# Performance work log

Hardware: AMD Instinct MI355X
Metric: run time of the kernel (lower is better)

Reference implementation:

```python
import jax, jax.numpy as jnp
import numpy as np

N = 200000   # nodes
E = 6400000  # edges (avg degree 32)
D = 128      # input feature dim
H = 10       # hidden dim (hardcoded in module)


def setup_inputs() -> dict:
    key = jax.random.key(0)
    ks = jax.random.split(key, 16)
    x = jax.random.normal(ks[0], (N, D), dtype=jnp.float32)
    edge_index = jax.random.randint(ks[1], (2, E), 0, N, dtype=jnp.int32)

    def lin(k, fan_in, fan_out):
        s = 1.0 / np.sqrt(fan_in)
        k1, k2 = jax.random.split(k)
        W = jax.random.uniform(k1, (fan_in, fan_out), jnp.float32, -s, s)
        b = jax.random.uniform(k2, (fan_out,), jnp.float32, -s, s)
        return W, b

    W1, b1 = lin(ks[2], D, H)    # conv_succ1
    W2, b2 = lin(ks[3], H, H)    # conv_succ2
    Wp, bp = lin(ks[4], H, H)    # conv_pred1
    W3, b3 = lin(ks[5], H, H)    # conv_succ3
    Wo, bo = lin(ks[6], H, 1)    # conv_probs (conv_output)
    Wdn, bdn = lin(ks[7], H, 1)  # do_nothing
    Wv, bv = lin(ks[8], H, 1)    # value
    return {"x": x, "edge_index": edge_index,
            "W1": W1, "b1": b1, "W2": W2, "b2": b2,
            "Wp": Wp, "bp": bp, "W3": W3, "b3": b3,
            "Wo": Wo, "bo": bo, "Wdn": Wdn, "bdn": bdn,
            "Wv": Wv, "bv": bv}


def gcn_conv(x, W, b, j, i, n):
    """PyG GCNConv: h = x@W; add self-loops; deg from aggregation index i;
    out[i] += deg^-1/2[i] * deg^-1/2[j] * h[j]; plus bias."""
    h = x @ W                                   # [n, out]
    loops = jnp.arange(n, dtype=j.dtype)
    jj = jnp.concatenate([j, loops])
    ii = jnp.concatenate([i, loops])
    deg = jax.ops.segment_sum(jnp.ones(ii.shape[0], x.dtype), ii, num_segments=n)
    dinv = jnp.where(deg > 0, jax.lax.rsqrt(deg), 0.0)
    norm = dinv[ii] * dinv[jj]                  # [E+n]
    out = jax.ops.segment_sum(norm[:, None] * h[jj], ii, num_segments=n)
    return out + b


def reference(x, edge_index, W1, b1, W2, b2, Wp, bp, W3, b3, Wo, bo, Wdn, bdn, Wv, bv):
    n = x.shape[0]
    row, col = edge_index[0], edge_index[1]
    # flow='target_to_source': message from col, aggregate at row
    h = jax.nn.relu(gcn_conv(x, W1, b1, col, row, n))
    h = jax.nn.relu(gcn_conv(h, W2, b2, col, row, n))
    # conv_pred1: default flow='source_to_target': message from row, aggregate at col
    h = jax.nn.relu(gcn_conv(h, Wp, bp, row, col, n))
    h = jax.nn.relu(gcn_conv(h, W3, b3, col, row, n))
    probs = gcn_conv(h, Wo, bo, col, row, n)[:, 0]   # [n]
    x_mean = jnp.mean(h, axis=0)                     # [H]
    v = x_mean @ Wv + bv                             # [1]
    prob_nothing = x_mean @ Wdn + bdn                # [1]
    probs = jnp.concatenate([probs, prob_nothing])   # [n+1]
    return probs, v
```

## Files before the change

### kernel.cpp

```cpp
#include <hip/hip_runtime.h>
#include <hip/hip_fp16.h>
#include <cstdio>

constexpr int NPB = 512;
constexpr int BSH = 9;
constexpr int BIN_CHUNK = 8192;
constexpr int CAP = 18432;

__device__ __forceinline__ int4 pack10(const float o[10]) {
  float mx = fabsf(o[0]);
#pragma unroll
  for (int k = 1; k < 10; ++k) mx = fmaxf(mx, fabsf(o[k]));
  int4 r;
  if (mx < 1e-30f) { r.x = 0; r.y = 0; r.z = 0; r.w = 0; return r; }
  int ebits = (__float_as_int(mx) >> 23) & 0xFF;
  if (ebits < 11) ebits = 11;
  float senc = __int_as_float((264 - ebits) << 23);
  int m[10];
#pragma unroll
  for (int k = 0; k < 10; ++k) {
    int v = (int)rintf(o[k] * senc);
    m[k] = min(2047, max(-2047, v));
  }
  int u8 = m[8] & 0xFFF, u9 = m[9] & 0xFFF;
  int e8 = ebits - 10;
  r.x = (m[0] & 0xFFF) | ((m[1] & 0xFFF) << 16) | ((u8 & 0xF) << 12) | (((u8 >> 4) & 0xF) << 28);
  r.y = (m[2] & 0xFFF) | ((m[3] & 0xFFF) << 16) | (((u8 >> 8) & 0xF) << 12) | ((u9 & 0xF) << 28);
  r.z = (m[4] & 0xFFF) | ((m[5] & 0xFFF) << 16) | (((u9 >> 4) & 0xF) << 12) | (((u9 >> 8) & 0xF) << 28);
  r.w = (m[6] & 0xFFF) | ((m[7] & 0xFFF) << 16) | ((e8 & 0xF) << 12) | (((e8 >> 4) & 0xF) << 28);
  return r;
}

__device__ __forceinline__ void unpack10_acc(int4 v, float acc[10]) {
  int e8 = ((v.w >> 12) & 0xF) | (((v.w >> 28) & 0xF) << 4);
  float s = __int_as_float(e8 << 23);
  int d[4] = {v.x, v.y, v.z, v.w};
#pragma unroll
  for (int j = 0; j < 4; ++j) {
    int lo = (d[j] << 20) >> 20;
    int hi = (d[j] << 4) >> 20;
    acc[2 * j] = fmaf((float)lo, s, acc[2 * j]);
    acc[2 * j + 1] = fmaf((float)hi, s, acc[2 * j + 1]);
  }
  int m8 = ((v.x >> 12) & 0xF) | (((v.x >> 28) & 0xF) << 4) | (((v.y >> 12) & 0xF) << 8);
  m8 = (m8 << 20) >> 20;
  int m9 = ((v.y >> 28) & 0xF) | (((v.z >> 12) & 0xF) << 4) | (((v.z >> 28) & 0xF) << 8);
  m9 = (m9 << 20) >> 20;
  acc[8] = fmaf((float)m8, s, acc[8]);
  acc[9] = fmaf((float)m9, s, acc[9]);
}

__device__ __forceinline__ void unpack10(int4 v, float o[10]) {
#pragma unroll
  for (int k = 0; k < 10; ++k) o[k] = 0.f;
  unpack10_acc(v, o);
}


__global__ __launch_bounds__(256) void k_histpb(const int* __restrict__ dst, int* __restrict__ hist,
                                                int E, int nblocks, int nbuck) {
  __shared__ int h[512];
  int t = threadIdx.x;
  h[t] = 0;
  h[t + 256] = 0;
  __syncthreads();
  int e0 = blockIdx.x * BIN_CHUNK + t;
  int eend = min(E, (blockIdx.x + 1) * BIN_CHUNK);
  for (int e = e0; e < eend; e += 256) atomicAdd(&h[dst[e] >> BSH], 1);
  __syncthreads();
  for (int b = t; b < nbuck; b += 256) hist[(size_t)b * nblocks + blockIdx.x] = h[b];
}

__global__ __launch_bounds__(256) void k_scanA(const int* __restrict__ in, int* __restrict__ out,
                                               int* __restrict__ bsum, int n) {
  int base = blockIdx.x * 2048 + threadIdx.x * 8;
  int v[8];
  int run = 0;
#pragma unroll
  for (int i = 0; i < 8; ++i) { int idx = base + i; v[i] = (idx < n) ? in[idx] : 0; }
#pragma unroll
  for (int i = 0; i < 8; ++i) { int t = v[i]; v[i] = run; run += t; }
  __shared__ int s[256];
  s[threadIdx.x] = run;
  __syncthreads();
  for (int off = 1; off < 256; off <<= 1) {
    int t = (threadIdx.x >= off) ? s[threadIdx.x - off] : 0;
    __syncthreads();
    s[threadIdx.x] += t;
    __syncthreads();
  }
  int toff = s[threadIdx.x] - run;
#pragma unroll
  for (int i = 0; i < 8; ++i) { int idx = base + i; if (idx < n) out[idx] = v[i] + toff; }
  if (threadIdx.x == 255) bsum[blockIdx.x] = s[255];
}

__global__ __launch_bounds__(1024) void k_scanB(int* bsum, int nb) {
  __shared__ int s[1024];
  int t = threadIdx.x;
  int v = (t < nb) ? bsum[t] : 0;
  s[t] = v;
  __syncthreads();
  for (int off = 1; off < 1024; off <<= 1) {
    int tv = (t >= off) ? s[t - off] : 0;
    __syncthreads();
    s[t] += tv;
    __syncthreads();
  }
  if (t < nb) bsum[t] = s[t] - v;
}

__global__ __launch_bounds__(256) void k_scanC(int* __restrict__ out, const int* __restrict__ bsum,
                                               int n, int total) {
  int base = blockIdx.x * 2048 + threadIdx.x * 8;
  int add = bsum[blockIdx.x];
#pragma unroll
  for (int i = 0; i < 8; ++i) { int idx = base + i; if (idx < n) out[idx] += add; }
  if (blockIdx.x == 0 && threadIdx.x == 0) out[n] = total;
}

__global__ __launch_bounds__(512) void k_binR(const int* __restrict__ dst, const int* __restrict__ src,
                                              const int* __restrict__ hist_s, int* __restrict__ bin,
                                              int E, int nblocks, int nbuck) {
  __shared__ int lbuf[BIN_CHUNK];
  __shared__ int ls[512];
  __shared__ int cur[512];
  __shared__ int gbase[512];
  int t = threadIdx.x;
  cur[t] = 0;
  __syncthreads();
  int blk0 = blockIdx.x * BIN_CHUNK;
  int eend = min(E, blk0 + BIN_CHUNK);
  int nent = eend - blk0;
  for (int e = blk0 + t; e < eend; e += 512) atomicAdd(&cur[dst[e] >> BSH], 1);
  __syncthreads();
  int v = cur[t];
  ls[t] = v;
  __syncthreads();
  for (int off = 1; off < 512; off <<= 1) {
    int x = (t >= off) ? ls[t - off] : 0;
    __syncthreads();
    ls[t] += x;
    __syncthreads();
  }
  int excl = ls[t] - v;
  __syncthreads();
  ls[t] = excl;
  cur[t] = excl;
  gbase[t] = (t < nbuck) ? hist_s[(size_t)t * nblocks + blockIdx.x] : 0;
  __syncthreads();
  for (int e = blk0 + t; e < eend; e += 512) {
    int d = dst[e];
    int slot = atomicAdd(&cur[d >> BSH], 1);
    lbuf[slot] = ((d & (NPB - 1)) << 18) | src[e];
  }
  __syncthreads();
  for (int i = t; i < nent; i += 512) {
    int w = lbuf[i];
    int lo = 0;
#pragma unroll
    for (int sh = 256; sh > 0; sh >>= 1) {
      int mid = lo + sh;
      if (mid < 512 && ls[mid] <= i) lo = mid;
    }
    __builtin_nontemporal_store(w, &bin[gbase[lo] + (i - ls[lo])]);
  }
}

__global__ __launch_bounds__(1024) void k_buildcsr(const int* __restrict__ bin, const int* __restrict__ hist_s,
                                                   int* __restrict__ rowptr, int* __restrict__ csr,
                                                   float* __restrict__ dinv, int N, int Etot, int nblocks) {
  __shared__ int cnt[NPB];
  __shared__ int sc[NPB];
  __shared__ int lbuf[CAP];
  int t = threadIdx.x;
  int b = blockIdx.x;
  int node0 = b << BSH;
  int nn = min(NPB, N - node0);
  int ebeg = hist_s[(size_t)b * nblocks];
  int eend = hist_s[(size_t)(b + 1) * nblocks];
  if (t < NPB) cnt[t] = (t < nn) ? 1 : 0;
  __syncthreads();
  for (int p = ebeg + t; p < eend; p += 1024)
    atomicAdd(&cnt[__builtin_nontemporal_load(&bin[p]) >> 18], 1);
  __syncthreads();
  int v = 0;
  if (t < NPB) { v = cnt[t]; sc[t] = v; }
  __syncthreads();
  for (int off = 1; off < NPB; off <<= 1) {
    int x = (t >= off && t < NPB) ? sc[t - off] : 0;
    __syncthreads();
    if (t < NPB) sc[t] += x;
    __syncthreads();
  }
  int excl = (t < NPB) ? (sc[t] - v) : 0;
  int cbase = ebeg + node0;
  if (t < nn) {
    rowptr[node0 + t] = cbase + excl;
    dinv[node0 + t] = rsqrtf((float)v);
  }
  int total2 = (eend - ebeg) + nn;
  bool stage = (total2 <= CAP);
  __syncthreads();
  if (t < NPB) cnt[t] = excl + ((t < nn) ? 1 : 0);
  if (t < nn) {
    if (stage) lbuf[excl] = node0 + t;
    else       csr[cbase + excl] = node0 + t;
  }
  __syncthreads();
  for (int p = ebeg + t; p < eend; p += 1024) {
    int w = __builtin_nontemporal_load(&bin[p]);
    int slot = atomicAdd(&cnt[w >> 18], 1);
    if (stage) lbuf[slot] = w & 0x3FFFF;
    else       csr[cbase + slot] = w & 0x3FFFF;
  }
  __syncthreads();
  if (stage)
    for (int i = t; i < total2; i += 1024)
      __builtin_nontemporal_store(lbuf[i], &csr[cbase + i]);
  if (b == 0 && t == 0) rowptr[N] = Etot + N;
}

__global__ __launch_bounds__(256) void k_xw(const float* __restrict__ x, const float* __restrict__ W1,
                                            const float* __restrict__ dinv, int4* __restrict__ tA, int n) {
  int tid = blockIdx.x * 256 + threadIdx.x;
  int sub = tid & 15;
  int rowStart = tid >> 4;
  int rowStride = (gridDim.x * 256) >> 4;
  float w[8][10];
#pragma unroll
  for (int jj = 0; jj < 8; ++jj)
#pragma unroll
    for (int k = 0; k < 10; ++k) w[jj][k] = W1[(sub * 8 + jj) * 10 + k];
  for (int row = rowStart; row < n; row += rowStride) {
    const float* xr = x + (size_t)row * 128 + sub * 8;
    float4 a = *(const float4*)xr;
    float4 b = *(const float4*)(xr + 4);
    float xv[8] = {a.x, a.y, a.z, a.w, b.x, b.y, b.z, b.w};
    float acc[10];
#pragma unroll
    for (int k = 0; k < 10; ++k) acc[k] = 0.f;
#pragma unroll
    for (int jj = 0; jj < 8; ++jj)
#pragma unroll
      for (int k = 0; k < 10; ++k) acc[k] = fmaf(xv[jj], w[jj][k], acc[k]);
#pragma unroll
    for (int off = 1; off < 16; off <<= 1)
#pragma unroll
      for (int k = 0; k < 10; ++k) acc[k] += __shfl_xor(acc[k], off);
    if (sub == 0) {
      float d = dinv[row];
      float o[10];
#pragma unroll
      for (int k = 0; k < 10; ++k) o[k] = acc[k] * d;
      tA[row] = pack10(o);
    }
  }
}

template <bool USE_W>
__global__ __launch_bounds__(256) void k_agg10(const int4* __restrict__ tin, int4* __restrict__ tout,
                                               const int* __restrict__ csr, const int* __restrict__ rowptr,
                                               const float* __restrict__ dinv_d, const float* __restrict__ dnext,
                                               const float* __restrict__ W, const float* __restrict__ bias,
                                               int n) {
  int tid = blockIdx.x * 256 + threadIdx.x;
  int q = tid >> 4, lane = tid & 15;
  if (q >= n) return;
  int beg = rowptr[q], end = rowptr[q + 1];
  float acc[10];
#pragma unroll
  for (int k = 0; k < 10; ++k) acc[k] = 0.f;
  for (int p = beg + lane; p < end; p += 16) {
    int src = __builtin_nontemporal_load(&csr[p]);
    int4 a = tin[src];
    unpack10_acc(a, acc);
  }
#pragma unroll
  for (int off = 1; off < 16; off <<= 1)
#pragma unroll
    for (int k = 0; k < 10; ++k) acc[k] += __shfl_xor(acc[k], off);
  float o = 0.f;
  if (lane < 10) {
    float dd = dinv_d[q];
    float dn = dnext[q];
    o = bias[lane];
    if (USE_W) {
#pragma unroll
      for (int m = 0; m < 10; ++m) o = fmaf(acc[m] * dd, W[m * 10 + lane], o);
    } else {
      o += acc[lane] * dd;
    }
    o = fmaxf(o, 0.f) * dn;
  }
  int l = threadIdx.x & 63;
  int qbase = l & 48;
  float oj[10];
#pragma unroll
  for (int k = 0; k < 10; ++k) oj[k] = __shfl(o, qbase + k, 64);
  if (lane == 0) tout[q] = pack10(oj);
}

__global__ __launch_bounds__(256) void k_agg1(const float* __restrict__ t5, float* __restrict__ probs,
                                              const int* __restrict__ csr, const int* __restrict__ rowptr,
                                              const float* __restrict__ dinv, const float* __restrict__ bo,
                                              int n) {
  int tid = blockIdx.x * 256 + threadIdx.x;
  int q = tid >> 4, lane = tid & 15;
  if (q >= n) return;
  int beg = rowptr[q], end = rowptr[q + 1];
  float acc = 0.f;
  for (int p = beg + lane; p < end; p += 16) acc += t5[__builtin_nontemporal_load(&csr[p])];
#pragma unroll
  for (int off = 1; off < 16; off <<= 1) acc += __shfl_xor(acc, off);
  if (lane == 0) probs[q] = fmaf(dinv[q], acc, bo[0]);
}

__global__ __launch_bounds__(256) void k_t5mean(const int4* __restrict__ tA, const float* __restrict__ Wo,
                                                const float* __restrict__ dinv, float* __restrict__ t5,
                                                float* __restrict__ part, int n) {
  int tid = blockIdx.x * 256 + threadIdx.x;
  float wo[10];
#pragma unroll
  for (int k = 0; k < 10; ++k) wo[k] = Wo[k];
  float p[10];
#pragma unroll
  for (int k = 0; k < 10; ++k) p[k] = 0.f;
  for (int rowi = tid; rowi < n; rowi += 128 * 256) {
    int4 a = tA[rowi];
    float hv[10];
    unpack10(a, hv);
    float s = 0.f;
#pragma unroll
    for (int k = 0; k < 10; ++k) s = fmaf(hv[k], wo[k], s);
    t5[rowi] = s;
    float inv = 1.0f / dinv[rowi];
#pragma unroll
    for (int k = 0; k < 10; ++k) p[k] = fmaf(hv[k], inv, p[k]);
  }
#pragma unroll
  for (int off = 1; off < 64; off <<= 1)
#pragma unroll
    for (int k = 0; k < 10; ++k) p[k] += __shfl_xor(p[k], off);
  __shared__ float sp[4][10];
  int w = threadIdx.x >> 6, ln = threadIdx.x & 63;
  if (ln == 0) {
#pragma unroll
    for (int k = 0; k < 10; ++k) sp[w][k] = p[k];
  }
  __syncthreads();
  if (threadIdx.x < 10)
    part[blockIdx.x * 10 + threadIdx.x] =
        sp[0][threadIdx.x] + sp[1][threadIdx.x] + sp[2][threadIdx.x] + sp[3][threadIdx.x];
}

__global__ void k_finish(const float* __restrict__ part, const float* __restrict__ Wdn,
                         const float* __restrict__ bdn, const float* __restrict__ Wv,
                         const float* __restrict__ bv, float* __restrict__ out, int n, int nPart) {
  __shared__ float m[10];
  int t = threadIdx.x;
  if (t < 10) {
    float s = 0.f;
    for (int b = 0; b < nPart; ++b) s += part[b * 10 + t];
    m[t] = s / (float)n;
  }
  __syncthreads();
  if (t == 0) {
    float pn = bdn[0], vv = bv[0];
    for (int k = 0; k < 10; ++k) {
      pn = fmaf(m[k], Wdn[k], pn);
      vv = fmaf(m[k], Wv[k], vv);
    }
    out[n] = pn;
    out[n + 1] = vv;
  }
}

extern "C" void kernel_launch(void* const* d_in, const int* in_sizes, int n_in,
                              void* d_out, int out_size, void* d_ws, size_t ws_size,
                              hipStream_t stream) {
  const float* x  = (const float*)d_in[0];
  const int* ei   = (const int*)d_in[1];
  const float* W1 = (const float*)d_in[2];
  const float* b1 = (const float*)d_in[3];
  const float* W2 = (const float*)d_in[4];
  const float* b2 = (const float*)d_in[5];
  const float* Wp = (const float*)d_in[6];
  const float* bp = (const float*)d_in[7];
  const float* W3 = (const float*)d_in[8];
  const float* b3 = (const float*)d_in[9];
  const float* Wo = (const float*)d_in[10];
  const float* bo = (const float*)d_in[11];
  const float* Wdn = (const float*)d_in[12];
  const float* bdn = (const float*)d_in[13];
  const float* Wv = (const float*)d_in[14];
  const float* bv = (const float*)d_in[15];

  int N = in_sizes[0] / 128;
  int E = in_sizes[1] / 2;
  const int* row = ei;
  const int* colv = ei + E;
  float* out = (float*)d_out;
  int nbuck = (N + NPB - 1) >> BSH;
  int bb = (E + BIN_CHUNK - 1) / BIN_CHUNK;
  size_t M = (size_t)nbuck * bb;

  char* ws = (char*)d_ws;
  size_t off = 0;
  auto alloc = [&](size_t b) -> void* {
    void* p = ws + off;
    off += (b + 255) & ~(size_t)255;
    return p;
  };
  int* csr_r = (int*)alloc((size_t)(E + N) * 4);
  int* csr_c = (int*)alloc((size_t)(E + N) * 4);
  int* rp_r = (int*)alloc((size_t)(N + 1) * 4);
  int* rp_c = (int*)alloc((size_t)(N + 1) * 4);
  float* dinv_r = (float*)alloc((size_t)N * 4);
  float* dinv_c = (float*)alloc((size_t)N * 4);
  int* hist = (int*)alloc((M + 1) * 4);
  int* bsum = (int*)alloc(4096);
  size_t binB = (size_t)E * 4;
  size_t tB_ = (size_t)N * 36 + 8192;
  char* region = (char*)alloc(binB > tB_ ? binB : tB_);
  int* bin = (int*)region;
  int4* tA_a = (int4*)region;
  int4* tA_b = (int4*)(region + (size_t)N * 16);
  float* t5  = (float*)(region + (size_t)N * 32);
  float* part = (float*)(region + (size_t)N * 36);
  if (off > ws_size) {
    fprintf(stderr, "WS too small: need %zu have %zu\n", off, ws_size);
    return;
  }

  int sb2 = (int)((M + 2047) / 2048);
  int ab = (int)(((size_t)N * 16 + 255) / 256);

  k_histpb<<<bb, 256, 0, stream>>>(row, hist, E, bb, nbuck);
  k_scanA<<<sb2, 256, 0, stream>>>(hist, hist, bsum, (int)M);
  k_scanB<<<1, 1024, 0, stream>>>(bsum, sb2);
  k_scanC<<<sb2, 256, 0, stream>>>(hist, bsum, (int)M, E);
  k_binR<<<bb, 512, 0, stream>>>(row, colv, hist, bin, E, bb, nbuck);
  k_buildcsr<<<nbuck, 1024, 0, stream>>>(bin, hist, rp_r, csr_r, dinv_r, N, E, bb);
  k_histpb<<<bb, 256, 0, stream>>>(colv, hist, E, bb, nbuck);
  k_scanA<<<sb2, 256, 0, stream>>>(hist, hist, bsum, (int)M);
  k_scanB<<<1, 1024, 0, stream>>>(bsum, sb2);
  k_scanC<<<sb2, 256, 0, stream>>>(hist, bsum, (int)M, E);
  k_binR<<<bb, 512, 0, stream>>>(colv, row, hist, bin, E, bb, nbuck);
  k_buildcsr<<<nbuck, 1024, 0, stream>>>(bin, hist, rp_c, csr_c, dinv_c, N, E, bb);

  k_xw<<<2048, 256, 0, stream>>>(x, W1, dinv_r, tA_a, N);
  k_agg10<false><<<ab, 256, 0, stream>>>(tA_a, tA_b, csr_r, rp_r, dinv_r, dinv_r, nullptr, b1, N);
  k_agg10<true><<<ab, 256, 0, stream>>>(tA_b, tA_a, csr_r, rp_r, dinv_r, dinv_c, W2, b2, N);
  k_agg10<true><<<ab, 256, 0, stream>>>(tA_a, tA_b, csr_c, rp_c, dinv_c, dinv_r, Wp, bp, N);
  k_agg10<true><<<ab, 256, 0, stream>>>(tA_b, tA_a, csr_r, rp_r, dinv_r, dinv_r, W3, b3, N);
  k_t5mean<<<128, 256, 0, stream>>>(tA_a, Wo, dinv_r, t5, part, N);
  k_agg1<<<ab, 256, 0, stream>>>(t5, out, csr_r, rp_r, dinv_r, bo, N);
  k_finish<<<1, 64, 0, stream>>>(part, Wdn, bdn, Wv, bv, out, N, 128);
}
```

Measured before the change: 478.0 us.

## Fuse row/col histograms and scans, enlarge bin chunks, unroll gather loops

Builds both the row and column bucket histograms in one kernel and runs a single scan over the concatenated histogram, cutting one histogram pass and one scan chain. The second binning and CSR build subtract E so offsets stay relative to the shared scan. Binning chunks double to 16384 edges with 1024-thread blocks, which doubles the shared-memory staging buffer. The aggregation loops are unrolled by two with plain loads in place of nontemporal ones, to put more gathers in flight.

```diff
diff --git a/kernel.cpp b/kernel.cpp
--- a/kernel.cpp
+++ b/kernel.cpp
@@ -4,7 +4,7 @@
 
 constexpr int NPB = 512;
 constexpr int BSH = 9;
-constexpr int BIN_CHUNK = 8192;
+constexpr int BIN_CHUNK = 16384;
 constexpr int CAP = 18432;
 
 __device__ __forceinline__ int4 pack10(const float o[10]) {
@@ -57,18 +57,23 @@
 }
 
 
-__global__ __launch_bounds__(256) void k_histpb(const int* __restrict__ dst, int* __restrict__ hist,
-                                                int E, int nblocks, int nbuck) {
-  __shared__ int h[512];
+__global__ __launch_bounds__(1024) void k_histpb2(const int* __restrict__ rowv, const int* __restrict__ colv,
+                                                  int* __restrict__ hist, int E, int nblocks, int nbuck, int M) {
+  __shared__ int hr[512], hc[512];
   int t = threadIdx.x;
-  h[t] = 0;
-  h[t + 256] = 0;
-  __syncthreads();
-  int e0 = blockIdx.x * BIN_CHUNK + t;
-  int eend = min(E, (blockIdx.x + 1) * BIN_CHUNK);
-  for (int e = e0; e < eend; e += 256) atomicAdd(&h[dst[e] >> BSH], 1);
-  __syncthreads();
-  for (int b = t; b < nbuck; b += 256) hist[(size_t)b * nblocks + blockIdx.x] = h[b];
+  if (t < 512) { hr[t] = 0; hc[t] = 0; }
+  __syncthreads();
+  int blk0 = blockIdx.x * BIN_CHUNK;
+  int eend = min(E, blk0 + BIN_CHUNK);
+  for (int e = blk0 + t; e < eend; e += 1024) {
+    atomicAdd(&hr[rowv[e] >> BSH], 1);
+    atomicAdd(&hc[colv[e] >> BSH], 1);
+  }
+  __syncthreads();
+  if (t < nbuck) {
+    hist[(size_t)t * nblocks + blockIdx.x] = hr[t];
+    hist[M + (size_t)t * nblocks + blockIdx.x] = hc[t];
+  }
 }
 
 __global__ __launch_bounds__(256) void k_scanA(const int* __restrict__ in, int* __restrict__ out,
@@ -119,43 +124,44 @@
   if (blockIdx.x == 0 && threadIdx.x == 0) out[n] = total;
 }
 
-__global__ __launch_bounds__(512) void k_binR(const int* __restrict__ dst, const int* __restrict__ src,
-                                              const int* __restrict__ hist_s, int* __restrict__ bin,
-                                              int E, int nblocks, int nbuck) {
+__global__ __launch_bounds__(1024) void k_binR(const int* __restrict__ dst, const int* __restrict__ src,
+                                               const int* __restrict__ hist_s, int* __restrict__ bin,
+                                               int E, int nblocks, int nbuck, int sub) {
   __shared__ int lbuf[BIN_CHUNK];
   __shared__ int ls[512];
   __shared__ int cur[512];
   __shared__ int gbase[512];
   int t = threadIdx.x;
-  cur[t] = 0;
+  if (t < 512) cur[t] = 0;
   __syncthreads();
   int blk0 = blockIdx.x * BIN_CHUNK;
   int eend = min(E, blk0 + BIN_CHUNK);
   int nent = eend - blk0;
-  for (int e = blk0 + t; e < eend; e += 512) atomicAdd(&cur[dst[e] >> BSH], 1);
-  __syncthreads();
-  int v = cur[t];
-  ls[t] = v;
+  for (int e = blk0 + t; e < eend; e += 1024) atomicAdd(&cur[dst[e] >> BSH], 1);
+  __syncthreads();
+  int v = (t < 512) ? cur[t] : 0;
+  if (t < 512) ls[t] = v;
   __syncthreads();
   for (int off = 1; off < 512; off <<= 1) {
-    int x = (t >= off) ? ls[t - off] : 0;
-    __syncthreads();
-    ls[t] += x;
-    __syncthreads();
-  }
-  int excl = ls[t] - v;
-  __syncthreads();
-  ls[t] = excl;
-  cur[t] = excl;
-  gbase[t] = (t < nbuck) ? hist_s[(size_t)t * nblocks + blockIdx.x] : 0;
-  __syncthreads();
-  for (int e = blk0 + t; e < eend; e += 512) {
+    int x = (t >= off && t < 512) ? ls[t - off] : 0;
+    __syncthreads();
+    if (t < 512) ls[t] += x;
+    __syncthreads();
+  }
+  if (t < 512) {
+    int excl = ls[t] - v;
+    ls[t] = excl;
+    cur[t] = excl;
+    gbase[t] = (t < nbuck) ? (hist_s[(size_t)t * nblocks + blockIdx.x] - sub) : 0;
+  }
+  __syncthreads();
+  for (int e = blk0 + t; e < eend; e += 1024) {
     int d = dst[e];
     int slot = atomicAdd(&cur[d >> BSH], 1);
     lbuf[slot] = ((d & (NPB - 1)) << 18) | src[e];
   }
   __syncthreads();
-  for (int i = t; i < nent; i += 512) {
+  for (int i = t; i < nent; i += 1024) {
     int w = lbuf[i];
     int lo = 0;
 #pragma unroll
@@ -169,7 +175,8 @@
 
 __global__ __launch_bounds__(1024) void k_buildcsr(const int* __restrict__ bin, const int* __restrict__ hist_s,
                                                    int* __restrict__ rowptr, int* __restrict__ csr,
-                                                   float* __restrict__ dinv, int N, int Etot, int nblocks) {
+                                                   float* __restrict__ dinv, int N, int Etot, int nblocks,
+                                                   int sub) {
   __shared__ int cnt[NPB];
   __shared__ int sc[NPB];
   __shared__ int lbuf[CAP];
@@ -177,12 +184,11 @@
   int b = blockIdx.x;
   int node0 = b << BSH;
   int nn = min(NPB, N - node0);
-  int ebeg = hist_s[(size_t)b * nblocks];
-  int eend = hist_s[(size_t)(b + 1) * nblocks];
+  int ebeg = hist_s[(size_t)b * nblocks] - sub;
+  int eend = hist_s[(size_t)(b + 1) * nblocks] - sub;
   if (t < NPB) cnt[t] = (t < nn) ? 1 : 0;
   __syncthreads();
-  for (int p = ebeg + t; p < eend; p += 1024)
-    atomicAdd(&cnt[__builtin_nontemporal_load(&bin[p]) >> 18], 1);
+  for (int p = ebeg + t; p < eend; p += 1024) atomicAdd(&cnt[bin[p] >> 18], 1);
   __syncthreads();
   int v = 0;
   if (t < NPB) { v = cnt[t]; sc[t] = v; }
@@ -209,7 +215,7 @@
   }
   __syncthreads();
   for (int p = ebeg + t; p < eend; p += 1024) {
-    int w = __builtin_nontemporal_load(&bin[p]);
+    int w = bin[p];
     int slot = atomicAdd(&cnt[w >> 18], 1);
     if (stage) lbuf[slot] = w & 0x3FFFF;
     else       csr[cbase + slot] = w & 0x3FFFF;
@@ -271,9 +277,17 @@
   float acc[10];
 #pragma unroll
   for (int k = 0; k < 10; ++k) acc[k] = 0.f;
-  for (int p = beg + lane; p < end; p += 16) {
-    int src = __builtin_nontemporal_load(&csr[p]);
-    int4 a = tin[src];
+  int p = beg + lane;
+  for (; p + 16 < end; p += 32) {
+    int s0 = csr[p];
+    int s1 = csr[p + 16];
+    int4 a0 = tin[s0];
+    int4 a1 = tin[s1];
+    unpack10_acc(a0, acc);
+    unpack10_acc(a1, acc);
+  }
+  if (p < end) {
+    int4 a = tin[csr[p]];
     unpack10_acc(a, acc);
   }
 #pragma unroll
@@ -310,7 +324,13 @@
   if (q >= n) return;
   int beg = rowptr[q], end = rowptr[q + 1];
   float acc = 0.f;
-  for (int p = beg + lane; p < end; p += 16) acc += t5[__builtin_nontemporal_load(&csr[p])];
+  int p = beg + lane;
+  for (; p + 16 < end; p += 32) {
+    float v0 = t5[csr[p]];
+    float v1 = t5[csr[p + 16]];
+    acc += v0 + v1;
+  }
+  if (p < end) acc += t5[csr[p]];
 #pragma unroll
   for (int off = 1; off < 16; off <<= 1) acc += __shfl_xor(acc, off);
   if (lane == 0) probs[q] = fmaf(dinv[q], acc, bo[0]);
@@ -404,6 +424,7 @@
   int nbuck = (N + NPB - 1) >> BSH;
   int bb = (E + BIN_CHUNK - 1) / BIN_CHUNK;
   size_t M = (size_t)nbuck * bb;
+  int n2 = (int)(2 * M);
 
   char* ws = (char*)d_ws;
   size_t off = 0;
@@ -418,7 +439,7 @@
   int* rp_c = (int*)alloc((size_t)(N + 1) * 4);
   float* dinv_r = (float*)alloc((size_t)N * 4);
   float* dinv_c = (float*)alloc((size_t)N * 4);
-  int* hist = (int*)alloc((M + 1) * 4);
+  int* hist = (int*)alloc((2 * M + 1) * 4);
   int* bsum = (int*)alloc(4096);
   size_t binB = (size_t)E * 4;
   size_t tB_ = (size_t)N * 36 + 8192;
@@ -433,21 +454,17 @@
     return;
   }
 
-  int sb2 = (int)((M + 2047) / 2048);
+  int sb2 = (n2 + 2047) / 2048;
   int ab = (int)(((size_t)N * 16 + 255) / 256);
 
-  k_histpb<<<bb, 256, 0, stream>>>(row, hist, E, bb, nbuck);
-  k_scanA<<<sb2, 256, 0, stream>>>(hist, hist, bsum, (int)M);
+  k_histpb2<<<bb, 1024, 0, stream>>>(row, colv, hist, E, bb, nbuck, (int)M);
+  k_scanA<<<sb2, 256, 0, stream>>>(hist, hist, bsum, n2);
   k_scanB<<<1, 1024, 0, stream>>>(bsum, sb2);
-  k_scanC<<<sb2, 256, 0, stream>>>(hist, bsum, (int)M, E);
-  k_binR<<<bb, 512, 0, stream>>>(row, colv, hist, bin, E, bb, nbuck);
-  k_buildcsr<<<nbuck, 1024, 0, stream>>>(bin, hist, rp_r, csr_r, dinv_r, N, E, bb);
-  k_histpb<<<bb, 256, 0, stream>>>(colv, hist, E, bb, nbuck);
-  k_scanA<<<sb2, 256, 0, stream>>>(hist, hist, bsum, (int)M);
-  k_scanB<<<1, 1024, 0, stream>>>(bsum, sb2);
-  k_scanC<<<sb2, 256, 0, stream>>>(hist, bsum, (int)M, E);
-  k_binR<<<bb, 512, 0, stream>>>(colv, row, hist, bin, E, bb, nbuck);
-  k_buildcsr<<<nbuck, 1024, 0, stream>>>(bin, hist, rp_c, csr_c, dinv_c, N, E, bb);
+  k_scanC<<<sb2, 256, 0, stream>>>(hist, bsum, n2, 2 * E);
+  k_binR<<<bb, 1024, 0, stream>>>(row, colv, hist, bin, E, bb, nbuck, 0);
+  k_buildcsr<<<nbuck, 1024, 0, stream>>>(bin, hist, rp_r, csr_r, dinv_r, N, E, bb, 0);
+  k_binR<<<bb, 1024, 0, stream>>>(colv, row, hist + M, bin, E, bb, nbuck, E);
+  k_buildcsr<<<nbuck, 1024, 0, stream>>>(bin, hist + M, rp_c, csr_c, dinv_c, N, E, bb, E);
 
   k_xw<<<2048, 256, 0, stream>>>(x, W1, dinv_r, tA_a, N);
   k_agg10<false><<<ab, 256, 0, stream>>>(tA_a, tA_b, csr_r, rp_r, dinv_r, dinv_r, nullptr, b1, N);
```

New measurement: 383.1 us. 19.9% less time.
